# Performance work log

Hardware: AMD Instinct MI355X
Metric: run time of the kernel (lower is better)

The kernel has to match this reference:

```python
import jax, jax.numpy as jnp
import numpy as np

B = 4096
N_PATCH = 196  # 14x14 patches of a 28x28 image
THRESHOLD = 0.9
SECONDARY = 0.5
SECONDARY_WEIGHT = 0.5

_CNOT = jnp.array([[1, 0, 0, 0], [0, 1, 0, 0], [0, 0, 0, 1], [0, 0, 1, 0]], dtype=jnp.complex64)


def _ry(t):
    c, s = jnp.cos(t / 2), jnp.sin(t / 2)
    m = jnp.stack([jnp.stack([c, -s], -1), jnp.stack([s, c], -1)], -2)
    return m.astype(jnp.complex64)


def _rx(t):
    c, s = jnp.cos(t / 2), jnp.sin(t / 2)
    z = jnp.zeros_like(c)
    re = jnp.stack([jnp.stack([c, z], -1), jnp.stack([z, c], -1)], -2)
    im = jnp.stack([jnp.stack([z, -s], -1), jnp.stack([-s, z], -1)], -2)
    return (re + 1j * im).astype(jnp.complex64)


def _rz(t):
    em = jnp.exp(-0.5j * t.astype(jnp.complex64) if hasattr(t, 'astype') else -0.5j * t)
    ep = jnp.conj(em)
    z = jnp.zeros_like(em)
    m = jnp.stack([jnp.stack([em, z], -1), jnp.stack([z, ep], -1)], -2)
    return m.astype(jnp.complex64)


def _apply_1q(state, mat, wire):
    # state: (P, 2, 2, 2, 2); mat: (2,2) shared or (P,2,2) per-sample
    s = jnp.moveaxis(state, 1 + wire, -1)
    if mat.ndim == 2:
        s = jnp.einsum('pabcj,ij->pabci', s, mat)
    else:
        s = jnp.einsum('pabcj,pij->pabci', s, mat)
    return jnp.moveaxis(s, -1, 1 + wire)


def _apply_2q(state, mat4, w0, w1):
    s = jnp.moveaxis(state, (1 + w0, 1 + w1), (-2, -1))
    shp = s.shape
    s = s.reshape(shp[:-2] + (4,))
    s = jnp.einsum('...j,ij->...i', s, mat4)
    return jnp.moveaxis(s.reshape(shp), (-2, -1), (1 + w0, 1 + w1))


def _quantum_measure(angles, q_params):
    # angles: (P, 4) real -> Pauli-Z expectations (P, 4)
    P = angles.shape[0]
    state = jnp.zeros((P, 2, 2, 2, 2), jnp.complex64).at[:, 0, 0, 0, 0].set(1.0)
    # GeneralEncoder: RY(pixel) on each wire
    for w in range(4):
        state = _apply_1q(state, _ry(angles[:, w]), w)
    # fixed 'RandomLayer' (8 ops, deterministic gate sequence, trainable params)
    state = _apply_1q(state, _rx(q_params[0]), 0)
    state = _apply_1q(state, _ry(q_params[1]), 1)
    state = _apply_1q(state, _rz(q_params[2]), 2)
    state = _apply_2q(state, _CNOT, 0, 1)
    state = _apply_1q(state, _rx(q_params[3]), 3)
    state = _apply_2q(state, _CNOT, 2, 3)
    state = _apply_1q(state, _ry(q_params[4]), 0)
    state = _apply_1q(state, _rz(q_params[5]), 3)
    probs = state.real ** 2 + state.imag ** 2
    exps = []
    for w in range(4):
        p = jnp.moveaxis(probs, 1 + w, 1)
        exps.append((p[:, 0] - p[:, 1]).reshape(P, -1).sum(-1))
    return jnp.stack(exps, -1)


def setup_inputs() -> dict:
    key = jax.random.key(0)
    k1, k2, k3, k4 = jax.random.split(key, 4)
    x = jax.random.uniform(k1, (B, 1, 28, 28), dtype=jnp.float32)
    q_params = jax.random.uniform(k2, (6,), dtype=jnp.float32) * 2.0 * np.pi
    W = jax.random.normal(k3, (10, 4 * 14 * 14), dtype=jnp.float32) * 0.03
    b = jax.random.normal(k4, (10,), dtype=jnp.float32) * 0.01
    return {"x": x, "q_params": q_params, "W": W, "b": b}


def reference(x, q_params, W, b):
    Bsz = x.shape[0]
    # extract 2x2 patches in (tl, tr, bl, br) order -> (B*196, 4)
    p = x[:, 0].reshape(Bsz, 14, 2, 14, 2)
    p = jnp.transpose(p, (0, 1, 3, 2, 4)).reshape(Bsz * N_PATCH, 4)
    meas = _quantum_measure(p, q_params).reshape(Bsz, N_PATCH, 4)
    # adjacency from cosine similarity of first sample's patch vectors
    v = meas[0]
    nrm = jnp.linalg.norm(v, axis=-1, keepdims=True)
    sim = (v @ v.T) / (nrm * nrm.T + 1e-12)
    adj = jnp.where(sim >= THRESHOLD, 1.0,
                    jnp.where(sim >= SECONDARY, SECONDARY_WEIGHT, 0.0)).astype(meas.dtype)
    agg = jnp.einsum('nm,bmd->bnd', adj, meas)
    logits = agg.reshape(Bsz, -1) @ W.T + b
    return jax.nn.log_softmax(logits, axis=-1)
```

## Files before the change

kernel.cpp:

```cpp
#include <hip/hip_runtime.h>
#include <hip/hip_bf16.h>


#define NP 196

__device__ __forceinline__ float quad3(const float* H, const float* wa,
                                       const float* wb) {
  return wa[0] * (H[0] * wb[0] + H[1] * wb[1] + H[2] * wb[2]) +
         wa[1] * (H[3] * wb[0] + H[4] * wb[1] + H[5] * wb[2]) +
         wa[2] * (H[6] * wb[0] + H[7] * wb[1] + H[8] * wb[2]);
}

__device__ __forceinline__ void build_H_all(const float* __restrict__ qp,
                                            float* __restrict__ H) {
  float qc[6], qs[6];
#pragma unroll
  for (int i = 0; i < 6; ++i) __sincosf(0.5f * qp[i], &qs[i], &qc[i]);
#pragma unroll
  for (int sub = 0; sub < 2; ++sub) {
    float Mr[4][4] = {}, Mi[4][4] = {};
    if (sub == 0) {
      Mr[0][0] = Mr[1][1] = Mr[2][2] = Mr[3][3] = qc[0];
      Mi[0][2] = Mi[2][0] = Mi[1][3] = Mi[3][1] = -qs[0];
#pragma unroll
      for (int j = 0; j < 4; ++j) {
        float a, b;
        a = Mr[0][j]; b = Mr[1][j]; Mr[0][j] = qc[1]*a - qs[1]*b; Mr[1][j] = qs[1]*a + qc[1]*b;
        a = Mi[0][j]; b = Mi[1][j]; Mi[0][j] = qc[1]*a - qs[1]*b; Mi[1][j] = qs[1]*a + qc[1]*b;
        a = Mr[2][j]; b = Mr[3][j]; Mr[2][j] = qc[1]*a - qs[1]*b; Mr[3][j] = qs[1]*a + qc[1]*b;
        a = Mi[2][j]; b = Mi[3][j]; Mi[2][j] = qc[1]*a - qs[1]*b; Mi[3][j] = qs[1]*a + qc[1]*b;
      }
#pragma unroll
      for (int j = 0; j < 4; ++j) {
        float r = Mr[2][j]; Mr[2][j] = Mr[3][j]; Mr[3][j] = r;
        float q = Mi[2][j]; Mi[2][j] = Mi[3][j]; Mi[3][j] = q;
      }
#pragma unroll
      for (int j = 0; j < 4; ++j) {
        float a, b;
        a = Mr[0][j]; b = Mr[2][j]; Mr[0][j] = qc[4]*a - qs[4]*b; Mr[2][j] = qs[4]*a + qc[4]*b;
        a = Mi[0][j]; b = Mi[2][j]; Mi[0][j] = qc[4]*a - qs[4]*b; Mi[2][j] = qs[4]*a + qc[4]*b;
        a = Mr[1][j]; b = Mr[3][j]; Mr[1][j] = qc[4]*a - qs[4]*b; Mr[3][j] = qs[4]*a + qc[4]*b;
        a = Mi[1][j]; b = Mi[3][j]; Mi[1][j] = qc[4]*a - qs[4]*b; Mi[3][j] = qs[4]*a + qc[4]*b;
      }
    } else {
      Mr[0][0] = Mr[1][1] = Mr[2][2] = Mr[3][3] = qc[2];
      Mi[0][0] = Mi[1][1] = -qs[2]; Mi[2][2] = Mi[3][3] = qs[2];
#pragma unroll
      for (int j = 0; j < 4; ++j) {
        float ra, ia, rb, ib;
        ra = Mr[0][j]; ia = Mi[0][j]; rb = Mr[1][j]; ib = Mi[1][j];
        Mr[0][j] = qc[3]*ra + qs[3]*ib;  Mi[0][j] = qc[3]*ia - qs[3]*rb;
        Mr[1][j] = qc[3]*rb + qs[3]*ia;  Mi[1][j] = qc[3]*ib - qs[3]*ra;
        ra = Mr[2][j]; ia = Mi[2][j]; rb = Mr[3][j]; ib = Mi[3][j];
        Mr[2][j] = qc[3]*ra + qs[3]*ib;  Mi[2][j] = qc[3]*ia - qs[3]*rb;
        Mr[3][j] = qc[3]*rb + qs[3]*ia;  Mi[3][j] = qc[3]*ib - qs[3]*ra;
      }
#pragma unroll
      for (int j = 0; j < 4; ++j) {
        float r = Mr[2][j]; Mr[2][j] = Mr[3][j]; Mr[3][j] = r;
        float q = Mi[2][j]; Mi[2][j] = Mi[3][j]; Mi[3][j] = q;
      }
#pragma unroll
      for (int r = 0; r < 4; ++r) {
        float sg = (r & 1) ? 1.0f : -1.0f;
#pragma unroll
        for (int j = 0; j < 4; ++j) {
          float re = Mr[r][j], im = Mi[r][j];
          Mr[r][j] = qc[5] * re - sg * qs[5] * im;
          Mi[r][j] = qc[5] * im + sg * qs[5] * re;
        }
      }
    }
#pragma unroll
    for (int d = 0; d < 2; ++d) {
      float G[4][4];
#pragma unroll
      for (int j = 0; j < 4; ++j)
#pragma unroll
        for (int k = 0; k < 4; ++k) {
          float g = 0.0f;
#pragma unroll
          for (int i = 0; i < 4; ++i) {
            float sg = (d == 0) ? ((i < 2) ? 1.f : -1.f)
                                : (((i & 1) == 0) ? 1.f : -1.f);
            g += sg * (Mr[i][j] * Mr[i][k] + Mi[i][j] * Mi[i][k]);
          }
          G[j][k] = g;
        }
      float* Hd = H + sub * 18 + d * 9;
      Hd[0] = G[0][0];       Hd[1] = 2.f * G[0][1];               Hd[2] = G[1][1];
      Hd[3] = 2.f * G[0][2]; Hd[4] = 2.f * (G[0][3] + G[1][2]);   Hd[5] = 2.f * G[1][3];
      Hd[6] = G[2][2];       Hd[7] = 2.f * G[2][3];               Hd[8] = G[3][3];
    }
  }
}

__device__ __forceinline__ void meas_patch(const float* __restrict__ xb, int p,
                                           const float* __restrict__ H,
                                           float* e) {
  int i = p / 14, j = p - 14 * i;
  float2 top = *(const float2*)(xb + 56 * i + 2 * j);
  float2 bot = *(const float2*)(xb + 56 * i + 28 + 2 * j);
  float c0, s0, c1, s1, c2, s2, c3, s3;
  __sincosf(0.5f * top.x, &s0, &c0);
  __sincosf(0.5f * top.y, &s1, &c1);
  __sincosf(0.5f * bot.x, &s2, &c2);
  __sincosf(0.5f * bot.y, &s3, &c3);
  float wA0[3] = {c0 * c0, c0 * s0, s0 * s0};
  float wA1[3] = {c1 * c1, c1 * s1, s1 * s1};
  float wB0[3] = {c2 * c2, c2 * s2, s2 * s2};
  float wB1[3] = {c3 * c3, c3 * s3, s3 * s3};
  e[0] = quad3(H, wA0, wA1);
  e[1] = quad3(H + 9, wA0, wA1);
  e[2] = quad3(H + 18, wB0, wB1);
  e[3] = quad3(H + 27, wB0, wB1);
}

__global__ __launch_bounds__(64, 1) void k_w2(const float* __restrict__ x,
                                              const float* __restrict__ qp,
                                              const float* __restrict__ W,
                                              float* __restrict__ W2,
                                              float* __restrict__ HG) {
  __shared__ float vs[NP][4];
  __shared__ float ns[NP];
  __shared__ float wrow[NP];
  int m = blockIdx.x, lane = threadIdx.x;

  float H[36];
  build_H_all(qp, H);

  if (m == 0 && lane == 0) {
#pragma unroll
    for (int i = 0; i < 36; ++i) HG[i] = H[i];
  }

#pragma unroll
  for (int r = 0; r < 4; ++r) {
    int p = lane + 64 * r;
    if (p < NP) {
      float e[4];
      meas_patch(x, p, H, e);
      vs[p][0] = e[0]; vs[p][1] = e[1]; vs[p][2] = e[2]; vs[p][3] = e[3];
      ns[p] = sqrtf(e[0]*e[0] + e[1]*e[1] + e[2]*e[2] + e[3]*e[3]);
    }
  }
  __syncthreads();
  float v0 = vs[m][0], v1 = vs[m][1], v2 = vs[m][2], v3 = vs[m][3];
  float nm = ns[m];
  for (int c = lane; c < NP; c += 64) {
    float dot = v0 * vs[c][0] + v1 * vs[c][1] + v2 * vs[c][2] + v3 * vs[c][3];
    float sim = dot / (nm * ns[c] + 1e-12f);
    wrow[c] = (sim >= 0.9f) ? 1.0f : ((sim >= 0.5f) ? 0.5f : 0.0f);
  }
  __syncthreads();
  if (lane < 40) {
    int k = lane >> 2, d = lane & 3;
    const float* Wk = W + k * 784 + d;
    float acc = 0.0f;
#pragma unroll 8
    for (int n = 0; n < NP; ++n) acc += wrow[n] * Wk[4 * n];
    W2[k * 784 + 4 * m + d] = acc;
  }
}

__global__ __launch_bounds__(256, 2) void k_main(const float* __restrict__ x,
                                                 const float* __restrict__ HG,
                                                 const float* __restrict__ bias,
                                                 const float* __restrict__ W2,
                                                 float* __restrict__ out,
                                                 int Bsz) {
  int t = threadIdx.x, wv = t >> 6, lane = t & 63;
  int b = blockIdx.x * 4 + wv;
  if (b >= Bsz) return;

  float H[36];
#pragma unroll
  for (int i = 0; i < 36; ++i) H[i] = HG[i];
  float bv[10];
#pragma unroll
  for (int k = 0; k < 10; ++k) bv[k] = bias[k];

  const float* xb = x + (size_t)b * 784;
  float acc[10];
#pragma unroll
  for (int k = 0; k < 10; ++k) acc[k] = 0.0f;

#pragma unroll
  for (int r = 0; r < 4; ++r) {
    int p = lane + 64 * r;
    if (p < NP) {
      float e[4];
      meas_patch(xb, p, H, e);
#pragma unroll
      for (int k = 0; k < 10; ++k) {
        float4 w = *(const float4*)(W2 + k * 784 + 4 * p);
        acc[k] += e[0] * w.x + e[1] * w.y + e[2] * w.z + e[3] * w.w;
      }
    }
  }
#pragma unroll
  for (int k = 0; k < 10; ++k)
#pragma unroll
    for (int off = 32; off; off >>= 1) acc[k] += __shfl_xor(acc[k], off);

  float lg[10], m = -1e30f;
#pragma unroll
  for (int k = 0; k < 10; ++k) { lg[k] = acc[k] + bv[k]; m = fmaxf(m, lg[k]); }
  float s = 0.0f;
#pragma unroll
  for (int k = 0; k < 10; ++k) s += __expf(lg[k] - m);
  float lse = m + __logf(s);
  if (lane < 10) {
    float sel = lg[0];
#pragma unroll
    for (int k = 1; k < 10; ++k) sel = (lane == k) ? lg[k] : sel;
    out[(size_t)b * 10 + lane] = sel - lse;
  }
}

extern "C" void kernel_launch(void* const* d_in, const int* in_sizes, int n_in,
                              void* d_out, int out_size, void* d_ws, size_t ws_size,
                              hipStream_t stream) {
  const float* x  = (const float*)d_in[0];
  const float* qp = (const float*)d_in[1];
  const float* W  = (const float*)d_in[2];
  const float* bi = (const float*)d_in[3];
  float* out = (float*)d_out;

  int Bsz = in_sizes[0] / 784;

  float* W2 = (float*)d_ws;
  float* HG = W2 + 7840;

  k_w2<<<NP, 64, 0, stream>>>(x, qp, W, W2, HG);
  k_main<<<(Bsz + 3) / 4, 256, 0, stream>>>(x, HG, bi, W2, out, Bsz);
}
```

Before: 93.19 us.

## Fuse adjacency construction and aggregation into a single per-batch kernel

Replaces the two-kernel scheme (precompute adjacency-folded weights W2, then main pass) with one kernel. Each block recomputes the normalized patch vectors of sample 0 and builds the 196x196 thresholded similarity on the fly. It aggregates each sample's measurements with that adjacency before applying W. This removes a launch and the W2 workspace dependency, but adds O(196^2) work per sample that was previously done once.

Measured after the change: 135.8 us. +45.7%, slower.

```diff
diff --git a/kernel.cpp b/kernel.cpp
--- a/kernel.cpp
+++ b/kernel.cpp
@@ -117,85 +117,70 @@
   e[3] = quad3(H + 27, wB0, wB1);
 }
 
-__global__ __launch_bounds__(64, 1) void k_w2(const float* __restrict__ x,
-                                              const float* __restrict__ qp,
-                                              const float* __restrict__ W,
-                                              float* __restrict__ W2,
-                                              float* __restrict__ HG) {
-  __shared__ float vs[NP][4];
-  __shared__ float ns[NP];
-  __shared__ float wrow[NP];
-  int m = blockIdx.x, lane = threadIdx.x;
+__global__ __launch_bounds__(256, 1) void k_fused(
+    const float* __restrict__ x, const float* __restrict__ qp,
+    const float* __restrict__ W, const float* __restrict__ bias,
+    float* __restrict__ out, int Bsz) {
+  __shared__ float4 us[NP];
+  __shared__ float4 ms[4][NP];
+  int t = threadIdx.x, wv = t >> 6, lane = t & 63;
+  int b = blockIdx.x * 4 + wv;
 
   float H[36];
   build_H_all(qp, H);
 
-  if (m == 0 && lane == 0) {
-#pragma unroll
-    for (int i = 0; i < 36; ++i) HG[i] = H[i];
-  }
-
-#pragma unroll
-  for (int r = 0; r < 4; ++r) {
-    int p = lane + 64 * r;
-    if (p < NP) {
-      float e[4];
-      meas_patch(x, p, H, e);
-      vs[p][0] = e[0]; vs[p][1] = e[1]; vs[p][2] = e[2]; vs[p][3] = e[3];
-      ns[p] = sqrtf(e[0]*e[0] + e[1]*e[1] + e[2]*e[2] + e[3]*e[3]);
-    }
-  }
-  __syncthreads();
-  float v0 = vs[m][0], v1 = vs[m][1], v2 = vs[m][2], v3 = vs[m][3];
-  float nm = ns[m];
-  for (int c = lane; c < NP; c += 64) {
-    float dot = v0 * vs[c][0] + v1 * vs[c][1] + v2 * vs[c][2] + v3 * vs[c][3];
-    float sim = dot / (nm * ns[c] + 1e-12f);
-    wrow[c] = (sim >= 0.9f) ? 1.0f : ((sim >= 0.5f) ? 0.5f : 0.0f);
-  }
-  __syncthreads();
-  if (lane < 40) {
-    int k = lane >> 2, d = lane & 3;
-    const float* Wk = W + k * 784 + d;
-    float acc = 0.0f;
-#pragma unroll 8
-    for (int n = 0; n < NP; ++n) acc += wrow[n] * Wk[4 * n];
-    W2[k * 784 + 4 * m + d] = acc;
-  }
-}
-
-__global__ __launch_bounds__(256, 2) void k_main(const float* __restrict__ x,
-                                                 const float* __restrict__ HG,
-                                                 const float* __restrict__ bias,
-                                                 const float* __restrict__ W2,
-                                                 float* __restrict__ out,
-                                                 int Bsz) {
-  int t = threadIdx.x, wv = t >> 6, lane = t & 63;
-  int b = blockIdx.x * 4 + wv;
-  if (b >= Bsz) return;
-
-  float H[36];
-#pragma unroll
-  for (int i = 0; i < 36; ++i) H[i] = HG[i];
-  float bv[10];
-#pragma unroll
-  for (int k = 0; k < 10; ++k) bv[k] = bias[k];
-
-  const float* xb = x + (size_t)b * 784;
-  float acc[10];
-#pragma unroll
-  for (int k = 0; k < 10; ++k) acc[k] = 0.0f;
-
+  if (t < NP) {
+    float e[4];
+    meas_patch(x, t, H, e);
+    float n = sqrtf(e[0]*e[0] + e[1]*e[1] + e[2]*e[2] + e[3]*e[3]) + 1e-12f;
+    float rn = 1.0f / n;
+    us[t] = make_float4(e[0]*rn, e[1]*rn, e[2]*rn, e[3]*rn);
+  }
+  bool alive = (b < Bsz);
+  const float* xb = x + (size_t)(alive ? b : 0) * 784;
 #pragma unroll
   for (int r = 0; r < 4; ++r) {
     int p = lane + 64 * r;
     if (p < NP) {
       float e[4];
       meas_patch(xb, p, H, e);
+      ms[wv][p] = make_float4(e[0], e[1], e[2], e[3]);
+    }
+  }
+  __syncthreads();
+
+  float4 un[4];
+  float4 agg[4];
+#pragma unroll
+  for (int r = 0; r < 4; ++r) {
+    int n = lane + 64 * r;
+    un[r] = (n < NP) ? us[n] : make_float4(0, 0, 0, 0);
+    agg[r] = make_float4(0, 0, 0, 0);
+  }
+  for (int m = 0; m < NP; ++m) {
+    float4 um = us[m];
+    float4 mm = ms[wv][m];
+#pragma unroll
+    for (int r = 0; r < 4; ++r) {
+      float dot = un[r].x*um.x + un[r].y*um.y + un[r].z*um.z + un[r].w*um.w;
+      float w = (dot >= 0.9f) ? 1.0f : ((dot >= 0.5f) ? 0.5f : 0.0f);
+      agg[r].x += w * mm.x; agg[r].y += w * mm.y;
+      agg[r].z += w * mm.z; agg[r].w += w * mm.w;
+    }
+  }
+
+  float acc[10];
+#pragma unroll
+  for (int k = 0; k < 10; ++k) acc[k] = 0.0f;
+#pragma unroll
+  for (int r = 0; r < 4; ++r) {
+    int n = lane + 64 * r;
+    if (n < NP) {
 #pragma unroll
       for (int k = 0; k < 10; ++k) {
-        float4 w = *(const float4*)(W2 + k * 784 + 4 * p);
-        acc[k] += e[0] * w.x + e[1] * w.y + e[2] * w.z + e[3] * w.w;
+        float4 w4 = *(const float4*)(W + k * 784 + 4 * n);
+        acc[k] += agg[r].x * w4.x + agg[r].y * w4.y +
+                  agg[r].z * w4.z + agg[r].w * w4.w;
       }
     }
   }
@@ -204,13 +189,14 @@
 #pragma unroll
     for (int off = 32; off; off >>= 1) acc[k] += __shfl_xor(acc[k], off);
 
-  float lg[10], m = -1e30f;
-#pragma unroll
-  for (int k = 0; k < 10; ++k) { lg[k] = acc[k] + bv[k]; m = fmaxf(m, lg[k]); }
-  float s = 0.0f;
-#pragma unroll
-  for (int k = 0; k < 10; ++k) s += __expf(lg[k] - m);
-  float lse = m + __logf(s);
+  if (!alive) return;
+  float lg[10], mx = -1e30f;
+#pragma unroll
+  for (int k = 0; k < 10; ++k) { lg[k] = acc[k] + bias[k]; mx = fmaxf(mx, lg[k]); }
+  float sm = 0.0f;
+#pragma unroll
+  for (int k = 0; k < 10; ++k) sm += __expf(lg[k] - mx);
+  float lse = mx + __logf(sm);
   if (lane < 10) {
     float sel = lg[0];
 #pragma unroll
@@ -230,9 +216,6 @@
 
   int Bsz = in_sizes[0] / 784;
 
-  float* W2 = (float*)d_ws;
-  float* HG = W2 + 7840;
-
-  k_w2<<<NP, 64, 0, stream>>>(x, qp, W, W2, HG);
-  k_main<<<(Bsz + 3) / 4, 256, 0, stream>>>(x, HG, bi, W2, out, Bsz);
-}
+  int grid = (Bsz + 3) / 4;
+  k_fused<<<grid, 256, 0, stream>>>(x, qp, W, bi, out, Bsz);
+}
```
